# Kernel optimization log

Hardware: AMD Instinct MI355X
Metric: run time of the kernel (lower is better)

Reference implementation:

```python
import jax, jax.numpy as jnp
import numpy as np

N = 100000
E = 1600000

def _gcn_layer(x, row, col, W, b):
    # gather neighbor feats then scatter-add into destination rows
    agg = jax.ops.segment_sum(x[col], row, num_segments=N)  # [N, d]
    deg = jax.ops.segment_sum(jnp.ones((row.shape[0],), x.dtype), row, num_segments=N)
    deg = jnp.clip(deg, 1.0, None)[:, None]  # [N, 1]
    return (agg / deg + x) @ W + b

def setup_inputs() -> dict:
    key = jax.random.key(0)
    ks = jax.random.split(key, 6)
    x = jax.random.normal(ks[0], (N, 64), dtype=jnp.float32)
    edge_index = jax.random.randint(ks[1], (2, E), 0, N, dtype=jnp.int64)
    W1 = jax.random.normal(ks[2], (64, 128), dtype=jnp.float32) * 0.1
    b1 = jax.random.normal(ks[3], (128,), dtype=jnp.float32) * 0.1
    W2 = jax.random.normal(ks[4], (128, 64), dtype=jnp.float32) * 0.1
    b2 = jax.random.normal(ks[5], (64,), dtype=jnp.float32) * 0.1
    return {"x": x, "edge_index": edge_index, "W1": W1, "b1": b1, "W2": W2, "b2": b2}

def reference(x, edge_index, W1, b1, W2, b2):
    row, col = edge_index[0], edge_index[1]
    h = jax.nn.relu(_gcn_layer(x, row, col, W1, b1))
    h = _gcn_layer(h, row, col, W2, b2)
    return h
```

## Files before the change

kernel.cpp:

```cpp
#include <hip/hip_runtime.h>
#include <stdint.h>

#define WS_ALIGN(x) (((x) + 255) & ~(size_t)255)
#define RPB 512
#define CAPB 9216

typedef __attribute__((ext_vector_type(8))) unsigned short ushort8_t;
typedef __attribute__((ext_vector_type(8))) short short8_t;
typedef __attribute__((ext_vector_type(4))) float float4_t;

static __device__ __forceinline__ unsigned short f2bf(float f) {
    unsigned u = __float_as_uint(f);
    unsigned r = (u + 0x7FFFu + ((u >> 16) & 1u)) >> 16;
    return (unsigned short)r;
}
static __device__ __forceinline__ float bf2f(unsigned short s) {
    return __uint_as_float(((unsigned)s) << 16);
}

__global__ __launch_bounds__(256) void prep_kernel(
    const float4* __restrict__ x, ushort4* __restrict__ xb, int n4,
    const float* __restrict__ W1, const float* __restrict__ W2,
    unsigned short* __restrict__ W1t, unsigned short* __restrict__ W2t,
    int* __restrict__ gCursor, int* __restrict__ gTotal, int nb) {
    int i = blockIdx.x * 256 + threadIdx.x;
    if (i < 8192) {
        int k = i >> 7, col = i & 127;
        W1t[col * 64 + k] = f2bf(W1[i]);
    } else if (i < 16384) {
        int j = i - 8192;
        int k = j >> 6, col = j & 63;
        W2t[col * 128 + k] = f2bf(W2[j]);
    }
    int c = i - 16384;
    if (c >= 0 && c < nb) gCursor[c] = c * CAPB;
    if (c == nb) *gTotal = 0;
    int j = i - (16384 + nb + 64);
    if (j >= 0 && j < n4 + 16) {
        ushort4 o = make_ushort4(0, 0, 0, 0);
        if (j < n4) {
            float4 f = x[j];
            o.x = f2bf(f.x); o.y = f2bf(f.y); o.z = f2bf(f.z); o.w = f2bf(f.w);
        }
        xb[j] = o;
    }
}

__global__ __launch_bounds__(256) void bucket_kernel(
    const void* __restrict__ eidx, int E,
    int nb, int* __restrict__ gCursor, int2* __restrict__ staging) {
    __shared__ int cnt[256];
    __shared__ int base[256];
    __shared__ int sOr;
    int t = threadIdx.x;
    if (t < nb) cnt[t] = 0;
    if (t == 0) sOr = 0;
    __syncthreads();

    int hv = 0;
    const int* p32 = (const int*)eidx;
    for (int i = t; i < 2048 && i < E; i += 256) hv |= p32[2 * i + 1];
    if (hv) atomicOr(&sOr, 1);
    __syncthreads();
    bool is64 = (sOr == 0);

    int e0 = (blockIdx.x * 256 + t) * 8;
    int m = E - e0; if (m > 8) m = 8; if (m < 0) m = 0;
    int r[8], bk[8], slot[8];
    for (int j = 0; j < m; ++j) {
        r[j] = is64 ? (int)((const long long*)eidx)[e0 + j]
                    : ((const int*)eidx)[e0 + j];
        bk[j] = r[j] >> 9;
        slot[j] = atomicAdd(&cnt[bk[j]], 1);
    }
    __syncthreads();
    if (t < nb) base[t] = cnt[t] ? atomicAdd(&gCursor[t], cnt[t]) : 0;
    __syncthreads();
    for (int j = 0; j < m; ++j) {
        int c = is64 ? (int)((const long long*)eidx)[E + e0 + j]
                     : ((const int*)eidx)[E + e0 + j];
        int dst = base[bk[j]] + slot[j];
        if (dst < (bk[j] + 1) * CAPB) staging[dst] = make_int2(r[j], c);
    }
}

__global__ __launch_bounds__(1024) void ell_kernel(
    const int2* __restrict__ staging, const int* __restrict__ gCursor,
    int* __restrict__ csr, int* __restrict__ deg, int* __restrict__ rowstart,
    int* __restrict__ gTotal, int N) {
    __shared__ int2 sd[CAPB];
    __shared__ int lcnt[RPB], scan[RPB], lcnt2[RPB];
    __shared__ int bucketBase;
    int b = blockIdx.x, t = threadIdx.x;
    if (t < RPB) { lcnt[t] = 0; lcnt2[t] = 0; }
    __syncthreads();

    int start = b * CAPB;
    int end = gCursor[b];
    if (end > start + CAPB) end = start + CAPB;
    int cnt = end - start;

    for (int i = t; i < cnt; i += 1024) {
        int2 rc = staging[start + i];
        sd[i] = rc;
        atomicAdd(&lcnt[rc.x & (RPB - 1)], 1);
    }
    __syncthreads();
    if (t < RPB) scan[t] = lcnt[t];
    __syncthreads();
    for (int off = 1; off < RPB; off <<= 1) {
        int v = 0;
        if (t < RPB && t >= off) v = scan[t - off];
        __syncthreads();
        if (t < RPB) scan[t] += v;
        __syncthreads();
    }
    if (t == 0) bucketBase = atomicAdd(gTotal, scan[RPB - 1]);
    __syncthreads();
    if (t < RPB) {
        int gr = (b << 9) + t;
        if (gr < N) {
            deg[gr] = lcnt[t];
            rowstart[gr] = bucketBase + scan[t] - lcnt[t];
        }
    }
    __syncthreads();
    for (int i = t; i < cnt; i += 1024) {
        int2 rc = sd[i];
        int lr = rc.x & (RPB - 1);
        int slot = atomicAdd(&lcnt2[lr], 1);
        csr[bucketBase + scan[lr] - lcnt[lr] + slot] = rc.y;
    }
}

__global__ __launch_bounds__(256) void agg_kernel(
    const unsigned short* __restrict__ xb, const int* __restrict__ deg,
    const int* __restrict__ rowstart, const int* __restrict__ csr,
    unsigned short* __restrict__ v, int N) {
    int tid = threadIdx.x;
    int w = tid >> 6, lane = tid & 63;
    int n = blockIdx.x * 4 + w;
    if (n >= N) return;
    int d = deg[n];
    if (d > 64) d = 64;
    int rp = rowstart[n];
    int ri = csr[rp + lane];
    if (lane >= d) ri = N;
    int nIter = __builtin_amdgcn_readfirstlane((d + 7) >> 3);

    float a0 = 0.f, a1 = 0.f, a2 = 0.f, a3 = 0.f;
#define GL(J, KK) const unsigned short* bp##J = \
        xb + ((size_t)(unsigned)__builtin_amdgcn_readlane(ri, (KK)) << 6); \
        unsigned short t##J = bp##J[lane];
    int it = 0;
    while (it < nIter) {
        int k0 = it * 8;
        if (nIter - it >= 2) {
            GL(0, k0 + 0)  GL(1, k0 + 1)  GL(2, k0 + 2)  GL(3, k0 + 3)
            GL(4, k0 + 4)  GL(5, k0 + 5)  GL(6, k0 + 6)  GL(7, k0 + 7)
            GL(8, k0 + 8)  GL(9, k0 + 9)  GL(10, k0 + 10) GL(11, k0 + 11)
            GL(12, k0 + 12) GL(13, k0 + 13) GL(14, k0 + 14) GL(15, k0 + 15)
            a0 += bf2f(t0) + bf2f(t4);   a1 += bf2f(t1) + bf2f(t5);
            a2 += bf2f(t2) + bf2f(t6);   a3 += bf2f(t3) + bf2f(t7);
            a0 += bf2f(t8) + bf2f(t12);  a1 += bf2f(t9) + bf2f(t13);
            a2 += bf2f(t10) + bf2f(t14); a3 += bf2f(t11) + bf2f(t15);
            it += 2;
        } else {
            GL(16, k0 + 0) GL(17, k0 + 1) GL(18, k0 + 2) GL(19, k0 + 3)
            GL(20, k0 + 4) GL(21, k0 + 5) GL(22, k0 + 6) GL(23, k0 + 7)
            a0 += bf2f(t16); a1 += bf2f(t17); a2 += bf2f(t18); a3 += bf2f(t19);
            a0 += bf2f(t20); a1 += bf2f(t21); a2 += bf2f(t22); a3 += bf2f(t23);
            it += 1;
        }
    }
#undef GL
    float a = (a0 + a1) + (a2 + a3);
    unsigned short s = xb[((size_t)n << 6) + lane];
    float inv = 1.0f / (float)(d > 1 ? d : 1);
    v[((size_t)n << 6) + lane] = f2bf(a * inv + bf2f(s));
}

__global__ __launch_bounds__(256) void mlp_kernel(
    const unsigned short* __restrict__ v, const unsigned short* __restrict__ W1t,
    const float* __restrict__ b1, const unsigned short* __restrict__ W2t,
    unsigned short* __restrict__ g16, int N) {
    __shared__ unsigned short hA[64 * 136];
    int t = threadIdx.x;
    int node0 = blockIdx.x * 64;
    int w = t >> 6, lane = t & 63;
    int l15 = lane & 15, quad = lane >> 4;
    const float4_t fzero = {0.f, 0.f, 0.f, 0.f};

    short8_t af[4][2];
    #pragma unroll
    for (int ms = 0; ms < 4; ++ms)
        #pragma unroll
        for (int kk = 0; kk < 2; ++kk)
            af[ms][kk] = *(const short8_t*)&v[(size_t)(node0 + ms * 16 + l15) * 64 + kk * 32 + quad * 8];
    short8_t bf1[2][2];
    #pragma unroll
    for (int cs = 0; cs < 2; ++cs)
        #pragma unroll
        for (int kk = 0; kk < 2; ++kk)
            bf1[cs][kk] = *(const short8_t*)&W1t[((w * 2 + cs) * 16 + l15) * 64 + kk * 32 + quad * 8];

    float4_t acc1[4][2];
    #pragma unroll
    for (int ms = 0; ms < 4; ++ms)
        #pragma unroll
        for (int cs = 0; cs < 2; ++cs)
            acc1[ms][cs] = fzero;
    #pragma unroll
    for (int ms = 0; ms < 4; ++ms)
        #pragma unroll
        for (int cs = 0; cs < 2; ++cs) {
            acc1[ms][cs] = __builtin_amdgcn_mfma_f32_16x16x32_bf16(af[ms][0], bf1[cs][0], acc1[ms][cs], 0, 0, 0);
            acc1[ms][cs] = __builtin_amdgcn_mfma_f32_16x16x32_bf16(af[ms][1], bf1[cs][1], acc1[ms][cs], 0, 0, 0);
        }

    #pragma unroll
    for (int cs = 0; cs < 2; ++cs) {
        int col = (w * 2 + cs) * 16 + l15;
        float bias = b1[col];
        #pragma unroll
        for (int ms = 0; ms < 4; ++ms) {
            #pragma unroll
            for (int r = 0; r < 4; ++r) {
                int node = ms * 16 + quad * 4 + r;
                hA[node * 136 + col] = f2bf(fmaxf(acc1[ms][cs][r] + bias, 0.f));
            }
        }
    }
    __syncthreads();

    short8_t bh[4];
    #pragma unroll
    for (int kk = 0; kk < 4; ++kk)
        bh[kk] = *(const short8_t*)&W2t[(w * 16 + l15) * 128 + kk * 32 + quad * 8];

    #pragma unroll
    for (int ms = 0; ms < 4; ++ms) {
        float4_t acc2 = fzero;
        #pragma unroll
        for (int kk = 0; kk < 4; ++kk) {
            short8_t ah = *(const short8_t*)&hA[(ms * 16 + l15) * 136 + kk * 32 + quad * 8];
            acc2 = __builtin_amdgcn_mfma_f32_16x16x32_bf16(ah, bh[kk], acc2, 0, 0, 0);
        }
        #pragma unroll
        for (int r = 0; r < 4; ++r) {
            int gn = node0 + ms * 16 + quad * 4 + r;
            if (gn < N) g16[(size_t)gn * 64 + w * 16 + l15] = f2bf(acc2[r]);
        }
    }
}

__global__ __launch_bounds__(256) void final_kernel(
    const unsigned short* __restrict__ g16, const float* __restrict__ b2,
    const int* __restrict__ deg, const int* __restrict__ rowstart,
    const int* __restrict__ csr, float* __restrict__ out, int N) {
    int tid = threadIdx.x;
    int w = tid >> 6, lane = tid & 63;
    int n = blockIdx.x * 4 + w;
    if (n >= N) return;
    int d = deg[n];
    if (d > 64) d = 64;
    int rp = rowstart[n];
    int ri = csr[rp + lane];
    if (lane >= d) ri = N;
    int nIter = __builtin_amdgcn_readfirstlane((d + 7) >> 3);

    float a0 = 0.f, a1 = 0.f, a2 = 0.f, a3 = 0.f;
#define GL(J, KK) const unsigned short* bp##J = \
        g16 + ((size_t)(unsigned)__builtin_amdgcn_readlane(ri, (KK)) << 6); \
        unsigned short t##J = bp##J[lane];
    int it = 0;
    while (it < nIter) {
        int k0 = it * 8;
        if (nIter - it >= 2) {
            GL(0, k0 + 0)  GL(1, k0 + 1)  GL(2, k0 + 2)  GL(3, k0 + 3)
            GL(4, k0 + 4)  GL(5, k0 + 5)  GL(6, k0 + 6)  GL(7, k0 + 7)
            GL(8, k0 + 8)  GL(9, k0 + 9)  GL(10, k0 + 10) GL(11, k0 + 11)
            GL(12, k0 + 12) GL(13, k0 + 13) GL(14, k0 + 14) GL(15, k0 + 15)
            a0 += bf2f(t0) + bf2f(t4);   a1 += bf2f(t1) + bf2f(t5);
            a2 += bf2f(t2) + bf2f(t6);   a3 += bf2f(t3) + bf2f(t7);
            a0 += bf2f(t8) + bf2f(t12);  a1 += bf2f(t9) + bf2f(t13);
            a2 += bf2f(t10) + bf2f(t14); a3 += bf2f(t11) + bf2f(t15);
            it += 2;
        } else {
            GL(16, k0 + 0) GL(17, k0 + 1) GL(18, k0 + 2) GL(19, k0 + 3)
            GL(20, k0 + 4) GL(21, k0 + 5) GL(22, k0 + 6) GL(23, k0 + 7)
            a0 += bf2f(t16); a1 += bf2f(t17); a2 += bf2f(t18); a3 += bf2f(t19);
            a0 += bf2f(t20); a1 += bf2f(t21); a2 += bf2f(t22); a3 += bf2f(t23);
            it += 1;
        }
    }
#undef GL
    float a = (a0 + a1) + (a2 + a3);
    unsigned short s = g16[((size_t)n << 6) + lane];
    float inv = 1.0f / (float)(d > 1 ? d : 1);
    out[((size_t)n << 6) + lane] = a * inv + bf2f(s) + b2[lane];
}

extern "C" void kernel_launch(void* const* d_in, const int* in_sizes, int n_in,
                              void* d_out, int out_size, void* d_ws, size_t ws_size,
                              hipStream_t stream) {
    const float* x  = (const float*)d_in[0];
    const void*  ei = d_in[1];
    const float* W1 = (const float*)d_in[2];
    const float* b1 = (const float*)d_in[3];
    const float* W2 = (const float*)d_in[4];
    const float* b2 = (const float*)d_in[5];
    float* out = (float*)d_out;

    int N = out_size / 64;
    int E = in_sizes[1] / 2;
    int nb = (N + RPB - 1) / RPB;

    char* ws = (char*)d_ws;
    size_t off = 0;
    auto alloc = [&](size_t bytes) { size_t r = off; off += WS_ALIGN(bytes); return r; };
    int* gTotal   = (int*)(ws + alloc(4));
    int* gCursor  = (int*)(ws + alloc((size_t)4 * nb));
    int* deg      = (int*)(ws + alloc((size_t)4 * N));
    int* rowstart = (int*)(ws + alloc((size_t)4 * N));
    int* csr      = (int*)(ws + alloc((size_t)4 * (E + 64)));
    char* bufA    = ws + alloc((size_t)128 * (N + 1));
    unsigned short* xb  = (unsigned short*)bufA;
    unsigned short* g16 = (unsigned short*)bufA;
    unsigned short* v   = (unsigned short*)(ws + alloc((size_t)128 * (N + 64)));
    unsigned short* W1t = (unsigned short*)(ws + alloc((size_t)2 * 8192));
    unsigned short* W2t = (unsigned short*)(ws + alloc((size_t)2 * 8192));
    int2* staging = (int2*)(ws + alloc((size_t)8 * nb * CAPB));
    (void)ws_size;

    int n4 = N * 16;
    int prepWork = 16384 + nb + 64 + n4 + 16;
    prep_kernel<<<(prepWork + 255) / 256, 256, 0, stream>>>(
        (const float4*)x, (ushort4*)xb, n4, W1, W2, W1t, W2t, gCursor, gTotal, nb);

    int b1blocks = (E + 2047) / 2048;
    bucket_kernel<<<b1blocks, 256, 0, stream>>>(ei, E, nb, gCursor, staging);
    ell_kernel<<<nb, 1024, 0, stream>>>(staging, gCursor, csr, deg, rowstart, gTotal, N);

    agg_kernel<<<(N + 3) / 4, 256, 0, stream>>>(xb, deg, rowstart, csr, v, N);
    mlp_kernel<<<(N + 63) / 64, 256, 0, stream>>>(v, W1t, b1, W2t, g16, N);
    final_kernel<<<(N + 3) / 4, 256, 0, stream>>>(g16, b2, deg, rowstart, csr, out, N);
}
```

Baseline: 244.6 us.

## Vectorize neighbor gathers: 16 lanes per row, 4 edges per wave load

Rewrites the gather loops in the aggregation and final kernels. Each lane now loads 8 bytes (4 bf16 features) instead of 2, so one wave instruction fetches four neighbor rows at once, using shuffles to pick the indices. Partial sums are then reduced across the four lane groups with xor-shuffles, and 16 lanes write the results with vector stores. The aim is fewer, wider memory instructions per edge, at the cost of cross-lane reductions and fewer edges in flight per loop iteration.

```diff
diff --git a/kernel.cpp b/kernel.cpp
--- a/kernel.cpp
+++ b/kernel.cpp
@@ -146,38 +146,42 @@
     int rp = rowstart[n];
     int ri = csr[rp + lane];
     if (lane >= d) ri = N;
-    int nIter = __builtin_amdgcn_readfirstlane((d + 7) >> 3);
+    int nq = __builtin_amdgcn_readfirstlane((d + 3) >> 2);
+    int lq = lane >> 4;
+    size_t loff = (size_t)((lane & 15) << 3);
+    const char* xbB = (const char*)xb;
 
     float a0 = 0.f, a1 = 0.f, a2 = 0.f, a3 = 0.f;
-#define GL(J, KK) const unsigned short* bp##J = \
-        xb + ((size_t)(unsigned)__builtin_amdgcn_readlane(ri, (KK)) << 6); \
-        unsigned short t##J = bp##J[lane];
-    int it = 0;
-    while (it < nIter) {
-        int k0 = it * 8;
-        if (nIter - it >= 2) {
-            GL(0, k0 + 0)  GL(1, k0 + 1)  GL(2, k0 + 2)  GL(3, k0 + 3)
-            GL(4, k0 + 4)  GL(5, k0 + 5)  GL(6, k0 + 6)  GL(7, k0 + 7)
-            GL(8, k0 + 8)  GL(9, k0 + 9)  GL(10, k0 + 10) GL(11, k0 + 11)
-            GL(12, k0 + 12) GL(13, k0 + 13) GL(14, k0 + 14) GL(15, k0 + 15)
-            a0 += bf2f(t0) + bf2f(t4);   a1 += bf2f(t1) + bf2f(t5);
-            a2 += bf2f(t2) + bf2f(t6);   a3 += bf2f(t3) + bf2f(t7);
-            a0 += bf2f(t8) + bf2f(t12);  a1 += bf2f(t9) + bf2f(t13);
-            a2 += bf2f(t10) + bf2f(t14); a3 += bf2f(t11) + bf2f(t15);
-            it += 2;
-        } else {
-            GL(16, k0 + 0) GL(17, k0 + 1) GL(18, k0 + 2) GL(19, k0 + 3)
-            GL(20, k0 + 4) GL(21, k0 + 5) GL(22, k0 + 6) GL(23, k0 + 7)
-            a0 += bf2f(t16); a1 += bf2f(t17); a2 += bf2f(t18); a3 += bf2f(t19);
-            a0 += bf2f(t20); a1 += bf2f(t21); a2 += bf2f(t22); a3 += bf2f(t23);
-            it += 1;
-        }
-    }
-#undef GL
-    float a = (a0 + a1) + (a2 + a3);
-    unsigned short s = xb[((size_t)n << 6) + lane];
-    float inv = 1.0f / (float)(d > 1 ? d : 1);
-    v[((size_t)n << 6) + lane] = f2bf(a * inv + bf2f(s));
+#define QL(J, Q) int rq##J = __shfl(ri, ((Q) << 2) + lq); \
+    uint2 u##J = *(const uint2*)(xbB + (((size_t)(unsigned)rq##J) << 7) + loff);
+#define QA(J) a0 += __uint_as_float(u##J.x << 16); \
+    a1 += __uint_as_float(u##J.x & 0xFFFF0000u); \
+    a2 += __uint_as_float(u##J.y << 16); \
+    a3 += __uint_as_float(u##J.y & 0xFFFF0000u);
+    int q = 0;
+    while (q + 4 <= nq) {
+        QL(0, q) QL(1, q + 1) QL(2, q + 2) QL(3, q + 3)
+        QA(0) QA(1) QA(2) QA(3)
+        q += 4;
+    }
+    while (q < nq) { QL(4, q) QA(4) ++q; }
+#undef QL
+#undef QA
+    a0 += __shfl_xor(a0, 16); a0 += __shfl_xor(a0, 32);
+    a1 += __shfl_xor(a1, 16); a1 += __shfl_xor(a1, 32);
+    a2 += __shfl_xor(a2, 16); a2 += __shfl_xor(a2, 32);
+    a3 += __shfl_xor(a3, 16); a3 += __shfl_xor(a3, 32);
+
+    if (lane < 16) {
+        uint2 su = *(const uint2*)(xbB + (((size_t)n) << 7) + loff);
+        float s0 = __uint_as_float(su.x << 16), s1 = __uint_as_float(su.x & 0xFFFF0000u);
+        float s2 = __uint_as_float(su.y << 16), s3 = __uint_as_float(su.y & 0xFFFF0000u);
+        float inv = 1.0f / (float)(d > 1 ? d : 1);
+        uint2 o;
+        o.x = (unsigned)f2bf(a0 * inv + s0) | ((unsigned)f2bf(a1 * inv + s1) << 16);
+        o.y = (unsigned)f2bf(a2 * inv + s2) | ((unsigned)f2bf(a3 * inv + s3) << 16);
+        *(uint2*)((char*)v + (((size_t)n) << 7) + loff) = o;
+    }
 }
 
 __global__ __launch_bounds__(256) void mlp_kernel(
@@ -267,38 +271,45 @@
     int rp = rowstart[n];
     int ri = csr[rp + lane];
     if (lane >= d) ri = N;
-    int nIter = __builtin_amdgcn_readfirstlane((d + 7) >> 3);
+    int nq = __builtin_amdgcn_readfirstlane((d + 3) >> 2);
+    int lq = lane >> 4;
+    size_t loff = (size_t)((lane & 15) << 3);
+    const char* gB = (const char*)g16;
 
     float a0 = 0.f, a1 = 0.f, a2 = 0.f, a3 = 0.f;
-#define GL(J, KK) const unsigned short* bp##J = \
-        g16 + ((size_t)(unsigned)__builtin_amdgcn_readlane(ri, (KK)) << 6); \
-        unsigned short t##J = bp##J[lane];
-    int it = 0;
-    while (it < nIter) {
-        int k0 = it * 8;
-        if (nIter - it >= 2) {
-            GL(0, k0 + 0)  GL(1, k0 + 1)  GL(2, k0 + 2)  GL(3, k0 + 3)
-            GL(4, k0 + 4)  GL(5, k0 + 5)  GL(6, k0 + 6)  GL(7, k0 + 7)
-            GL(8, k0 + 8)  GL(9, k0 + 9)  GL(10, k0 + 10) GL(11, k0 + 11)
-            GL(12, k0 + 12) GL(13, k0 + 13) GL(14, k0 + 14) GL(15, k0 + 15)
-            a0 += bf2f(t0) + bf2f(t4);   a1 += bf2f(t1) + bf2f(t5);
-            a2 += bf2f(t2) + bf2f(t6);   a3 += bf2f(t3) + bf2f(t7);
-            a0 += bf2f(t8) + bf2f(t12);  a1 += bf2f(t9) + bf2f(t13);
-            a2 += bf2f(t10) + bf2f(t14); a3 += bf2f(t11) + bf2f(t15);
-            it += 2;
-        } else {
-            GL(16, k0 + 0) GL(17, k0 + 1) GL(18, k0 + 2) GL(19, k0 + 3)
-            GL(20, k0 + 4) GL(21, k0 + 5) GL(22, k0 + 6) GL(23, k0 + 7)
-            a0 += bf2f(t16); a1 += bf2f(t17); a2 += bf2f(t18); a3 += bf2f(t19);
-            a0 += bf2f(t20); a1 += bf2f(t21); a2 += bf2f(t22); a3 += bf2f(t23);
-            it += 1;
-        }
-    }
-#undef GL
-    float a = (a0 + a1) + (a2 + a3);
-    unsigned short s = g16[((size_t)n << 6) + lane];
-    float inv = 1.0f / (float)(d > 1 ? d : 1);
-    out[((size_t)n << 6) + lane] = a * inv + bf2f(s) + b2[lane];
+#define QL(J, Q) int rq##J = __shfl(ri, ((Q) << 2) + lq); \
+    uint2 u##J = *(const uint2*)(gB + (((size_t)(unsigned)rq##J) << 7) + loff);
+#define QA(J) a0 += __uint_as_float(u##J.x << 16); \
+    a1 += __uint_as_float(u##J.x & 0xFFFF0000u); \
+    a2 += __uint_as_float(u##J.y << 16); \
+    a3 += __uint_as_float(u##J.y & 0xFFFF0000u);
+    int q = 0;
+    while (q + 4 <= nq) {
+        QL(0, q) QL(1, q + 1) QL(2, q + 2) QL(3, q + 3)
+        QA(0) QA(1) QA(2) QA(3)
+        q += 4;
+    }
+    while (q < nq) { QL(4, q) QA(4) ++q; }
+#undef QL
+#undef QA
+    a0 += __shfl_xor(a0, 16); a0 += __shfl_xor(a0, 32);
+    a1 += __shfl_xor(a1, 16); a1 += __shfl_xor(a1, 32);
+    a2 += __shfl_xor(a2, 16); a2 += __shfl_xor(a2, 32);
+    a3 += __shfl_xor(a3, 16); a3 += __shfl_xor(a3, 32);
+
+    if (lane < 16) {
+        uint2 su = *(const uint2*)(gB + (((size_t)n) << 7) + loff);
+        float s0 = __uint_as_float(su.x << 16), s1 = __uint_as_float(su.x & 0xFFFF0000u);
+        float s2 = __uint_as_float(su.y << 16), s3 = __uint_as_float(su.y & 0xFFFF0000u);
+        float4 bz = ((const float4*)b2)[lane & 15];
+        float inv = 1.0f / (float)(d > 1 ? d : 1);
+        float4 o;
+        o.x = a0 * inv + s0 + bz.x;
+        o.y = a1 * inv + s1 + bz.y;
+        o.z = a2 * inv + s2 + bz.z;
+        o.w = a3 * inv + s3 + bz.w;
+        *(float4*)((char*)out + (((size_t)n) << 8) + (loff << 1)) = o;
+    }
 }
 
 extern "C" void kernel_launch(void* const* d_in, const int* in_sizes, int n_in,
```

Measured after the change: 234.9 us (median of 2 runs). 1.04x faster.
